# Kernel tuning notes

Measured on AMD Instinct MI355X. Metric: run time of the kernel, lower is better.

## Reference

```python
import jax, jax.numpy as jnp
import numpy as np

NUM_GROUPS = 32
RANK = 64            # per-head rank (uniform)
IN_FEATURES = 4096
OUT_FEATURES = 4096
GROUP_DIM = OUT_FEATURES // NUM_GROUPS  # 128
SUM_RANKS = NUM_GROUPS * RANK           # 2048


def setup_inputs() -> dict:
    key = jax.random.key(0)
    k1, k2, k3 = jax.random.split(key, 3)
    hidden_states = jax.random.normal(k1, (4, 4096, IN_FEATURES), dtype=jnp.float32)
    # VT: nn.Linear(in_features, sum(ranks), bias=False) -> weight [sum_ranks, in]
    VT_weight = jax.random.normal(k2, (SUM_RANKS, IN_FEATURES), dtype=jnp.float32) * (1.0 / np.sqrt(IN_FEATURES))
    # U_list: per-group nn.Linear(r, group_dim), init.normal_ -> stacked [G, group_dim, r]
    U_weight = jax.random.normal(k3, (NUM_GROUPS, GROUP_DIM, RANK), dtype=jnp.float32)
    return {"hidden_states": hidden_states, "VT_weight": VT_weight, "U_weight": U_weight}


def reference(hidden_states, VT_weight, U_weight):
    # shared down-projection: [B,S,in] @ [in,sum_ranks] -> [B,S,sum_ranks]
    z = jnp.einsum('bsi,ri->bsr', hidden_states, VT_weight)
    B, S, _ = z.shape
    # grouped up-projection (block-diagonal GEMM): slice per group -> [B,S,G,r]
    zg = z.reshape(B, S, NUM_GROUPS, RANK)
    out = jnp.einsum('bsgr,gdr->bsgd', zg, U_weight)  # [B,S,G,group_dim]
    return out.reshape(B, S, NUM_GROUPS * GROUP_DIM)  # concat along last dim
```

## Files before the change

kernel.cpp:

```cpp
#include <hip/hip_runtime.h>
#include <hip/hip_bf16.h>
#include <stdint.h>

typedef __attribute__((ext_vector_type(8)))  short bf16x8;
typedef __attribute__((ext_vector_type(4)))  float f32x4;
typedef __attribute__((ext_vector_type(4)))  float float4v;
typedef __attribute__((ext_vector_type(8)))  unsigned short u16x8;

#define MFMA16(a,b,c) __builtin_amdgcn_mfma_f32_16x16x32_bf16((a),(b),(c),0,0,0)

__device__ __forceinline__ unsigned short f2bf(float f) {
    unsigned int u = __builtin_bit_cast(unsigned int, f);
    u = (u + 0x7fffu + ((u >> 16) & 1u)) >> 16;
    return (unsigned short)u;
}

__device__ __forceinline__ void gload_lds16(const void* g, void* l) {
    __builtin_amdgcn_global_load_lds(
        (const __attribute__((address_space(1))) void*)g,
        (__attribute__((address_space(3))) void*)l, 16, 0, 0);
}

template<int N> __device__ __forceinline__ void waitvm() {}
template<> __device__ __forceinline__ void waitvm<6>() { asm volatile("s_waitcnt vmcnt(6)" ::: "memory"); }
template<> __device__ __forceinline__ void waitvm<4>() { asm volatile("s_waitcnt vmcnt(4)" ::: "memory"); }
template<> __device__ __forceinline__ void waitvm<0>() { asm volatile("s_waitcnt vmcnt(0)" ::: "memory"); }

__global__ void cvt_all(const float* __restrict__ hs, const float* __restrict__ vt,
                        unsigned short* __restrict__ hs_bf, unsigned short* __restrict__ vt_bf) {
    if (blockIdx.x < 2048) {
        long i = ((long)blockIdx.x * blockDim.x + threadIdx.x) * 8;
        const long stride = 2048L * 256 * 8;
        for (; i < 67108864L; i += stride) {
            float4v v0 = *(const float4v*)(hs + i);
            float4v v1 = *(const float4v*)(hs + i + 4);
            u16x8 o;
            o[0] = f2bf(v0[0]); o[1] = f2bf(v0[1]); o[2] = f2bf(v0[2]); o[3] = f2bf(v0[3]);
            o[4] = f2bf(v1[0]); o[5] = f2bf(v1[1]); o[6] = f2bf(v1[2]); o[7] = f2bf(v1[3]);
            *(u16x8*)(hs_bf + i) = o;
        }
    } else {
        long i = ((long)(blockIdx.x - 2048) * blockDim.x + threadIdx.x) * 8;
        const long stride = 512L * 256 * 8;
        for (; i < 8388608L; i += stride) {
            float4v v0 = *(const float4v*)(vt + i);
            float4v v1 = *(const float4v*)(vt + i + 4);
            u16x8 o;
            o[0] = f2bf(v0[0]); o[1] = f2bf(v0[1]); o[2] = f2bf(v0[2]); o[3] = f2bf(v0[3]);
            o[4] = f2bf(v1[0]); o[5] = f2bf(v1[1]); o[6] = f2bf(v1[2]); o[7] = f2bf(v1[3]);
            *(u16x8*)(vt_bf + i) = o;
        }
    }
}


#define STAGE_A(nA_, k0n, h, l) \
    gload_lds16(pA + ((l)*128 + (h)*64) * 4096L + (k0n), (nA_) + dA0 + ((l)*128 + (h)*64) * 64)
#define STAGE_B(nB_, k0n, h, l) \
    gload_lds16(pB + ((l)*128 + (h)*32) * 4096L + (k0n), (nB_) + dB0 + ((l)*128 + (h)*32) * 64)

#define LDA(dst_, sA_, QM) do { _Pragma("unroll") for (int mi = 0; mi < 4; ++mi) { \
    dst_[mi][0] = *(const bf16x8*)((sA_) + ((wr*128 + (QM)*64 + mi*16 + lan15) << 6) + g0); \
    dst_[mi][1] = *(const bf16x8*)((sA_) + ((wr*128 + (QM)*64 + mi*16 + lan15) << 6) + (g0 ^ 32)); } } while (0)
#define LDB(dst_, sB_, QN) do { _Pragma("unroll") for (int ni = 0; ni < 2; ++ni) { \
    dst_[ni][0] = *(const bf16x8*)((sB_) + ((wc*64 + (QN)*32 + ni*16 + lan15) << 6) + g0); \
    dst_[ni][1] = *(const bf16x8*)((sB_) + ((wc*64 + (QN)*32 + ni*16 + lan15) << 6) + (g0 ^ 32)); } } while (0)

#define DOMFMA(QM, QN, aset_, bset_) do { __builtin_amdgcn_s_setprio(1); \
    _Pragma("unroll") for (int mi = 0; mi < 4; ++mi) \
      _Pragma("unroll") for (int ni = 0; ni < 2; ++ni) { \
        acc[(QM)*4+mi][(QN)*2+ni] = MFMA16(aset_[mi][0], bset_[ni][0], acc[(QM)*4+mi][(QN)*2+ni]); \
        acc[(QM)*4+mi][(QN)*2+ni] = MFMA16(aset_[mi][1], bset_[ni][1], acc[(QM)*4+mi][(QN)*2+ni]); } \
    __builtin_amdgcn_s_setprio(0); } while (0)

#define BARX() do { __builtin_amdgcn_s_barrier(); \
    asm volatile("s_waitcnt lgkmcnt(0)" ::: "memory"); \
    __builtin_amdgcn_sched_barrier(0); } while (0)
#define SB() __builtin_amdgcn_sched_barrier(0)

#define ITER8(K1, K2, K3, S2, S3, T8, V3, V7) do { \
   STAGE_A(bA1, K1, 1, 0); STAGE_A(bA1, K1, 1, 1); \
         BARX(); DOMFMA(0, 0, aE, b0); LDB(b1, bB0, 1); SB(); \
   BARX(); DOMFMA(0, 1, aE, b1); LDA(aO, bA0, 1); SB(); \
   if (S2) { STAGE_A(bA0, K2, 0, 0); STAGE_A(bA0, K2, 0, 1); \
                   STAGE_B(bB0, K2, 0, 0); STAGE_B(bB0, K2, 0, 1); } \
         BARX(); DOMFMA(1, 1, aO, b1); waitvm<V3>(); SB(); \
   if (S2) { STAGE_B(bB0, K2, 1, 0); STAGE_B(bB0, K2, 1, 1); } \
         BARX(); DOMFMA(1, 0, aO, b0); LDA(aE, bA1, 0); LDB(b0, bB1, 0); SB(); \
   if (S2) { STAGE_A(bA0, K2, 1, 0); STAGE_A(bA0, K2, 1, 1); } \
         BARX(); DOMFMA(0, 0, aE, b0); LDB(b1, bB1, 1); SB(); \
   BARX(); DOMFMA(0, 1, aE, b1); LDA(aO, bA1, 1); SB(); \
   if (S3) { STAGE_A(bA1, K3, 0, 0); STAGE_A(bA1, K3, 0, 1); \
                   STAGE_B(bB1, K3, 0, 0); STAGE_B(bB1, K3, 0, 1); } \
         BARX(); DOMFMA(1, 1, aO, b1); waitvm<V7>(); SB(); \
   if (S3) { STAGE_B(bB1, K3, 1, 0); STAGE_B(bB1, K3, 1, 1); } \
         BARX(); DOMFMA(1, 0, aO, b0); \
         if (T8) { LDA(aE, bA0, 0); LDB(b0, bB0, 0); } SB(); \
} while (0)

__global__ __launch_bounds__(512, 2) void gemm1_8ph(const unsigned short* __restrict__ A,
                                                    const unsigned short* __restrict__ B,
                                                    unsigned short* __restrict__ Z) {
    __shared__ __align__(16) unsigned short lds[65536];

    const int tid   = threadIdx.x;
    const int lane  = tid & 63;
    const int wid   = tid >> 6;
    const int wr    = wid >> 2;
    const int wc    = wid & 3;
    const int lan15 = lane & 15;
    const int g0    = (((lane >> 4) ^ (lane & 7)) << 3);

    const int  bid = blockIdx.x;
    const long m0  = (long)(bid >> 3) * 256;
    const long n0  = (long)(bid & 7) * 256;

    const int q8    = tid >> 3;
    const int granA = (((tid & 7) ^ (q8 & 7)) << 3);
    const unsigned short* pA = A + (m0 + q8) * 4096L + granA;
    const int rB0   = (q8 & 31) + ((q8 >> 5) << 6);
    const unsigned short* pB = B + (n0 + rB0) * 4096L + granA;
    const int dA0   = (wid * 8) * 64;
    const int dB0   = ((wid & 3) * 8 + ((wid >> 2) << 6)) * 64;

    f32x4 acc[8][4] = {};
    bf16x8 aE[4][2], aO[4][2], b0[2][2], b1[2][2];

    unsigned short* bA0 = lds;
    unsigned short* bB0 = lds + 16384;
    unsigned short* bA1 = lds + 32768;
    unsigned short* bB1 = lds + 49152;

    STAGE_A(bA0, 0, 0, 0);  STAGE_A(bA0, 0, 0, 1);
    STAGE_B(bB0, 0, 0, 0);  STAGE_B(bB0, 0, 0, 1);
    STAGE_B(bB0, 0, 1, 0);  STAGE_B(bB0, 0, 1, 1);
    STAGE_A(bA0, 0, 1, 0);  STAGE_A(bA0, 0, 1, 1);
    STAGE_A(bA1, 64, 0, 0); STAGE_A(bA1, 64, 0, 1);
    STAGE_B(bB1, 64, 0, 0); STAGE_B(bB1, 64, 0, 1);
    STAGE_B(bB1, 64, 1, 0); STAGE_B(bB1, 64, 1, 1);
    waitvm<6>();
    __builtin_amdgcn_s_barrier();
    __builtin_amdgcn_sched_barrier(0);
    LDA(aE, bA0, 0); LDB(b0, bB0, 0);
    SB();

    for (int i = 0; i < 31; ++i) {
        ITER8((2 * i + 1) * 64, (2 * i + 2) * 64, (2 * i + 3) * 64,
              true, true, true, 4, 4);
    }
    ITER8(63 * 64, 0, 0, false, false, false, 0, -1);

    const int rq = (lane >> 4) << 2;
    #pragma unroll
    for (int mi = 0; mi < 8; ++mi) {
        #pragma unroll
        for (int ni = 0; ni < 4; ++ni) {
            const long mb  = m0 + wr * 128 + mi * 16 + rq;
            const long nb2 = n0 + wc * 64 + ni * 16 + lan15;
            #pragma unroll
            for (int j = 0; j < 4; ++j)
                Z[(mb + j) * 2048L + nb2] = f2bf(acc[mi][ni][j]);
        }
    }
}

#define U_PAD 80

__global__ __launch_bounds__(256) void gemm2(const unsigned short* __restrict__ Z,
                                             const float* __restrict__ U,
                                             float* __restrict__ out) {
    __shared__ __align__(16) unsigned short lU[128 * U_PAD];

    const int tid  = threadIdx.x;
    const int lane = tid & 63;
    const int wid  = tid >> 6;
    const int g    = blockIdx.x & 31;
    const long m0  = (long)(blockIdx.x >> 5) * 64;

    const float* ug = U + (long)g * (128 * 64);
    for (int i = tid; i < (128 * 64) / 4; i += 256) {
        const int r = i >> 4;
        const int c = (i << 2) & 63;
        float4v v = *(const float4v*)(ug + i * 4);
        unsigned short* d = &lU[r * U_PAD + c];
        d[0] = f2bf(v[0]); d[1] = f2bf(v[1]); d[2] = f2bf(v[2]); d[3] = f2bf(v[3]);
    }
    __syncthreads();

    const long mrow = m0 + wid * 16 + (lane & 15);
    const unsigned short* zrow = Z + mrow * 2048L + g * 64 + ((lane >> 4) << 3);
    const bf16x8 a0 = *(const bf16x8*)(zrow);
    const bf16x8 a1 = *(const bf16x8*)(zrow + 32);

    f32x4 acc[8] = {};
    const int blds = (lane & 15);
    const int kofs = (lane >> 4) << 3;
    #pragma unroll
    for (int ni = 0; ni < 8; ++ni) {
        const bf16x8 c0 = *(const bf16x8*)&lU[(ni * 16 + blds) * U_PAD + kofs];
        const bf16x8 c1 = *(const bf16x8*)&lU[(ni * 16 + blds) * U_PAD + 32 + kofs];
        acc[ni] = MFMA16(a0, c0, acc[ni]);
        acc[ni] = MFMA16(a1, c1, acc[ni]);
    }

    const long mb = m0 + wid * 16 + ((lane >> 4) << 2);
    const long cb = (long)g * 128 + (lane & 15);
    #pragma unroll
    for (int ni = 0; ni < 8; ++ni)
        #pragma unroll
        for (int j = 0; j < 4; ++j)
            out[(mb + j) * 4096L + cb + ni * 16] = acc[ni][j];
}

extern "C" void kernel_launch(void* const* d_in, const int* in_sizes, int n_in,
                              void* d_out, int out_size, void* d_ws, size_t ws_size,
                              hipStream_t stream) {
    const float* hs = (const float*)d_in[0];
    const float* vt = (const float*)d_in[1];
    const float* uw = (const float*)d_in[2];
    float* out = (float*)d_out;

    unsigned short* hs_bf = (unsigned short*)d_ws;
    unsigned short* vt_bf = hs_bf + 67108864L;
    unsigned short* z_bf  = vt_bf + 8388608L;

    cvt_all<<<2560, 256, 0, stream>>>(hs, vt, hs_bf, vt_bf);

    gemm1_8ph<<<512, 512, 0, stream>>>(hs_bf, vt_bf, z_bf);

    gemm2<<<8192, 256, 0, stream>>>(z_bf, uw, out);
}
```

Before: 360.1 us.

## Restructure GEMM1 main loop from 8-phase to 4-phase pipeline

Replaces the 8-phase K-loop schedule in the first GEMM with a 4-phase schedule. Each phase now issues two quadrant MFMA blocks between barriers and loads both B fragments at once. The new schedule waits for all outstanding global-to-LDS loads (vmcnt 0) in most phases and no longer prefetches the second stage in the prologue. The aim is to halve barrier count per K step, at the cost of less overlap between global loads and MFMA work and more register pressure from holding both B fragments.

After: 375.0 us. 4.1% more time.

```diff
diff --git a/kernel.cpp b/kernel.cpp
--- a/kernel.cpp
+++ b/kernel.cpp
@@ -22,8 +22,6 @@
 }
 
 template<int N> __device__ __forceinline__ void waitvm() {}
-template<> __device__ __forceinline__ void waitvm<6>() { asm volatile("s_waitcnt vmcnt(6)" ::: "memory"); }
-template<> __device__ __forceinline__ void waitvm<4>() { asm volatile("s_waitcnt vmcnt(4)" ::: "memory"); }
 template<> __device__ __forceinline__ void waitvm<0>() { asm volatile("s_waitcnt vmcnt(0)" ::: "memory"); }
 
 __global__ void cvt_all(const float* __restrict__ hs, const float* __restrict__ vt,
@@ -66,39 +64,47 @@
     dst_[ni][0] = *(const bf16x8*)((sB_) + ((wc*64 + (QN)*32 + ni*16 + lan15) << 6) + g0); \
     dst_[ni][1] = *(const bf16x8*)((sB_) + ((wc*64 + (QN)*32 + ni*16 + lan15) << 6) + (g0 ^ 32)); } } while (0)
 
-#define DOMFMA(QM, QN, aset_, bset_) do { __builtin_amdgcn_s_setprio(1); \
+#define DOMFMA(QM, QN, aset_, bset_) do { \
     _Pragma("unroll") for (int mi = 0; mi < 4; ++mi) \
       _Pragma("unroll") for (int ni = 0; ni < 2; ++ni) { \
         acc[(QM)*4+mi][(QN)*2+ni] = MFMA16(aset_[mi][0], bset_[ni][0], acc[(QM)*4+mi][(QN)*2+ni]); \
         acc[(QM)*4+mi][(QN)*2+ni] = MFMA16(aset_[mi][1], bset_[ni][1], acc[(QM)*4+mi][(QN)*2+ni]); } \
-    __builtin_amdgcn_s_setprio(0); } while (0)
+    } while (0)
 
 #define BARX() do { __builtin_amdgcn_s_barrier(); \
     asm volatile("s_waitcnt lgkmcnt(0)" ::: "memory"); \
     __builtin_amdgcn_sched_barrier(0); } while (0)
 #define SB() __builtin_amdgcn_sched_barrier(0)
 
-#define ITER8(K1, K2, K3, S2, S3, T8, V3, V7) do { \
-   STAGE_A(bA1, K1, 1, 0); STAGE_A(bA1, K1, 1, 1); \
-         BARX(); DOMFMA(0, 0, aE, b0); LDB(b1, bB0, 1); SB(); \
-   BARX(); DOMFMA(0, 1, aE, b1); LDA(aO, bA0, 1); SB(); \
-   if (S2) { STAGE_A(bA0, K2, 0, 0); STAGE_A(bA0, K2, 0, 1); \
-                   STAGE_B(bB0, K2, 0, 0); STAGE_B(bB0, K2, 0, 1); } \
-         BARX(); DOMFMA(1, 1, aO, b1); waitvm<V3>(); SB(); \
-   if (S2) { STAGE_B(bB0, K2, 1, 0); STAGE_B(bB0, K2, 1, 1); } \
-         BARX(); DOMFMA(1, 0, aO, b0); LDA(aE, bA1, 0); LDB(b0, bB1, 0); SB(); \
-   if (S2) { STAGE_A(bA0, K2, 1, 0); STAGE_A(bA0, K2, 1, 1); } \
-         BARX(); DOMFMA(0, 0, aE, b0); LDB(b1, bB1, 1); SB(); \
-   BARX(); DOMFMA(0, 1, aE, b1); LDA(aO, bA1, 1); SB(); \
-   if (S3) { STAGE_A(bA1, K3, 0, 0); STAGE_A(bA1, K3, 0, 1); \
-                   STAGE_B(bB1, K3, 0, 0); STAGE_B(bB1, K3, 0, 1); } \
-         BARX(); DOMFMA(1, 1, aO, b1); waitvm<V7>(); SB(); \
-   if (S3) { STAGE_B(bB1, K3, 1, 0); STAGE_B(bB1, K3, 1, 1); } \
-         BARX(); DOMFMA(1, 0, aO, b0); \
-         if (T8) { LDA(aE, bA0, 0); LDB(b0, bB0, 0); } SB(); \
+#define ITER4(KV, KU2, SV, SU, TD, WC_, WD_) do { \
+   if (SV) { STAGE_A(bA1, KV, 0, 0); STAGE_A(bA1, KV, 0, 1); \
+                   STAGE_B(bB1, KV, 0, 0); STAGE_B(bB1, KV, 0, 1); \
+                   STAGE_B(bB1, KV, 1, 0); STAGE_B(bB1, KV, 1, 1); } \
+         BARX(); __builtin_amdgcn_s_setprio(1); \
+         DOMFMA(0, 0, aE, b0); DOMFMA(0, 1, aE, b1); \
+         __builtin_amdgcn_s_setprio(0); \
+         LDA(aO, bA0, 1); waitvm<0>(); SB(); \
+   if (SV) { STAGE_A(bA1, KV, 1, 0); STAGE_A(bA1, KV, 1, 1); } \
+         BARX(); __builtin_amdgcn_s_setprio(1); \
+         DOMFMA(1, 1, aO, b1); DOMFMA(1, 0, aO, b0); \
+         __builtin_amdgcn_s_setprio(0); \
+         LDA(aE, bA1, 0); LDB(b0, bB1, 0); LDB(b1, bB1, 1); waitvm<0>(); SB(); \
+   if (SU) { STAGE_A(bA0, KU2, 0, 0); STAGE_A(bA0, KU2, 0, 1); \
+                   STAGE_B(bB0, KU2, 0, 0); STAGE_B(bB0, KU2, 0, 1); \
+                   STAGE_B(bB0, KU2, 1, 0); STAGE_B(bB0, KU2, 1, 1); } \
+         BARX(); __builtin_amdgcn_s_setprio(1); \
+         DOMFMA(0, 0, aE, b0); DOMFMA(0, 1, aE, b1); \
+         __builtin_amdgcn_s_setprio(0); \
+         LDA(aO, bA1, 1); waitvm<WC_>(); SB(); \
+   if (SU) { STAGE_A(bA0, KU2, 1, 0); STAGE_A(bA0, KU2, 1, 1); } \
+         BARX(); __builtin_amdgcn_s_setprio(1); \
+         DOMFMA(1, 1, aO, b1); DOMFMA(1, 0, aO, b0); \
+         __builtin_amdgcn_s_setprio(0); \
+         if (TD) { LDA(aE, bA0, 0); LDB(b0, bB0, 0); LDB(b1, bB0, 1); } \
+         waitvm<WD_>(); SB(); \
 } while (0)
 
-__global__ __launch_bounds__(512, 2) void gemm1_8ph(const unsigned short* __restrict__ A,
+__global__ __launch_bounds__(512, 2) void gemm1_4ph(const unsigned short* __restrict__ A,
                                                     const unsigned short* __restrict__ B,
                                                     unsigned short* __restrict__ Z) {
     __shared__ __align__(16) unsigned short lds[65536];
@@ -135,20 +141,16 @@
     STAGE_B(bB0, 0, 0, 0);  STAGE_B(bB0, 0, 0, 1);
     STAGE_B(bB0, 0, 1, 0);  STAGE_B(bB0, 0, 1, 1);
     STAGE_A(bA0, 0, 1, 0);  STAGE_A(bA0, 0, 1, 1);
-    STAGE_A(bA1, 64, 0, 0); STAGE_A(bA1, 64, 0, 1);
-    STAGE_B(bB1, 64, 0, 0); STAGE_B(bB1, 64, 0, 1);
-    STAGE_B(bB1, 64, 1, 0); STAGE_B(bB1, 64, 1, 1);
-    waitvm<6>();
+    waitvm<0>();
     __builtin_amdgcn_s_barrier();
     __builtin_amdgcn_sched_barrier(0);
-    LDA(aE, bA0, 0); LDB(b0, bB0, 0);
+    LDA(aE, bA0, 0); LDB(b0, bB0, 0); LDB(b1, bB0, 1);
     SB();
 
-    for (int i = 0; i < 31; ++i) {
-        ITER8((2 * i + 1) * 64, (2 * i + 2) * 64, (2 * i + 3) * 64,
-              true, true, true, 4, 4);
-    }
-    ITER8(63 * 64, 0, 0, false, false, false, 0, -1);
+    for (int j = 0; j < 31; ++j) {
+        ITER4((2 * j + 1) * 64, (2 * j + 2) * 64, true, true, true, 0, 0);
+    }
+    ITER4(63 * 64, 0, true, false, false, 0, -1);
 
     const int rq = (lane >> 4) << 2;
     #pragma unroll
@@ -226,7 +228,7 @@
 
     cvt_all<<<2560, 256, 0, stream>>>(hs, vt, hs_bf, vt_bf);
 
-    gemm1_8ph<<<512, 512, 0, stream>>>(hs_bf, vt_bf, z_bf);
+    gemm1_4ph<<<512, 512, 0, stream>>>(hs_bf, vt_bf, z_bf);
 
     gemm2<<<8192, 256, 0, stream>>>(z_bf, uw, out);
 }
```
